# Performance work log

Measured on AMD Instinct MI355X. Metric: run time of the kernel, lower is better.

## Reference

```python
import jax, jax.numpy as jnp
import numpy as np

D_SPEC, D_PRE, D_CTX, D_H = 552, 256, 128, 1024


def _lstm_cell(x, h, c, Wih, Whh, bih, bhh):
    # PyTorch gate order: i, f, g, o
    g = x @ Wih.T + bih + h @ Whh.T + bhh
    i, f, gg, o = jnp.split(g, 4, axis=-1)
    c_new = jax.nn.sigmoid(f) * c + jax.nn.sigmoid(i) * jnp.tanh(gg)
    h_new = jax.nn.sigmoid(o) * jnp.tanh(c_new)
    return h_new, c_new


def _conv1d(x, w, b):
    # x: [B, C_in, L], w: [C_out, C_in, K], 'same' padding for K=5
    y = jax.lax.conv_general_dilated(x, w, window_strides=(1,), padding=[(2, 2)],
                                     dimension_numbers=('NCH', 'OIH', 'NCH'))
    return y + b[None, :, None]


def setup_inputs() -> dict:
    key = jax.random.key(0)
    ks = jax.random.split(key, 26)
    s = 0.05
    shapes = {
        'S_pad': (600, 64, D_SPEC),
        'pre_W1': (D_PRE, D_SPEC), 'pre_b1': (D_PRE,),
        'pre_W2': (D_PRE, D_PRE), 'pre_b2': (D_PRE,),
        'Wih0': (4 * D_H, D_PRE + D_CTX), 'Whh0': (4 * D_H, D_H),
        'bih0': (4 * D_H,), 'bhh0': (4 * D_H,),
        'Wih1': (4 * D_H, D_H), 'Whh1': (4 * D_H, D_H),
        'bih1': (4 * D_H,), 'bhh1': (4 * D_H,),
        'lin_W': (D_SPEC, D_H + D_CTX), 'lin_b': (D_SPEC,),
        'cw1': (512, D_SPEC, 5), 'cb1': (512,),
        'cw2': (512, 512, 5), 'cb2': (512,),
        'cw3': (512, 512, 5), 'cb3': (512,),
        'cw4': (512, 512, 5), 'cb4': (512,),
        'cw5': (D_SPEC, 512, 5), 'cb5': (D_SPEC,),
    }
    out = {}
    for i, (name, shp) in enumerate(shapes.items()):
        scale = 1.0 if name == 'S_pad' else s
        out[name] = scale * jax.random.normal(ks[i], shp, dtype=jnp.float32)
    return out


def reference(S_pad, pre_W1, pre_b1, pre_W2, pre_b2,
              Wih0, Whh0, bih0, bhh0, Wih1, Whh1, bih1, bhh1,
              lin_W, lin_b, cw1, cb1, cw2, cb2, cw3, cb3, cw4, cb4, cw5, cb5):
    L, B, _ = S_pad.shape
    # teacher forcing: input frame at t is S_pad[t-1] (zeros at t=0) -> precompute pre_net batched
    in_frames = jnp.concatenate([jnp.zeros((1, B, D_SPEC), S_pad.dtype), S_pad[:-1]], axis=0)
    pre = jax.nn.relu(in_frames @ pre_W1.T + pre_b1)
    pre = jax.nn.relu(pre @ pre_W2.T + pre_b2)  # dropout = identity (eval)
    ctx = jnp.zeros((L, B, D_CTX), S_pad.dtype)  # dummy_context
    lstm_in = jnp.concatenate([pre, ctx], axis=-1)  # [L, B, 384]

    h0 = jnp.zeros((B, D_H), S_pad.dtype)
    init = (h0, h0, h0, h0)  # (h0, c0, h1, c1)

    def step(carry, x):
        h0, c0, h1, c1 = carry
        h0, c0 = _lstm_cell(x, h0, c0, Wih0, Whh0, bih0, bhh0)
        h1, c1 = _lstm_cell(h0, h1, c1, Wih1, Whh1, bih1, bhh1)
        return (h0, c0, h1, c1), h1

    _, outs = jax.lax.scan(step, init, lstm_in)  # [L, B, 1024]
    S_pred = jnp.concatenate([outs, ctx], axis=-1) @ lin_W.T + lin_b  # [L, B, 552]

    x = jnp.transpose(S_pred, (1, 2, 0))  # [B, 552, L]
    x = jnp.tanh(_conv1d(x, cw1, cb1))
    x = jnp.tanh(_conv1d(x, cw2, cb2))
    x = jnp.tanh(_conv1d(x, cw3, cb3))
    x = jnp.tanh(_conv1d(x, cw4, cb4))
    x = _conv1d(x, cw5, cb5)
    S_residual = jnp.transpose(x, (2, 0, 1))  # [L, B, 552]
    return S_pred + S_residual
```

## Files before the change

kernel.cpp:

```cpp
#include <hip/hip_runtime.h>
#include <cstdint>
#include <cstddef>

typedef __bf16 bf16;
typedef __attribute__((ext_vector_type(8))) __bf16 bf16x8;
typedef __attribute__((ext_vector_type(4))) float f32x4;

#define DEV static __device__ __forceinline__

DEV float sigm_(float x) { return 1.f / (1.f + __expf(-x)); }
DEV float tanhf_(float x) {
  float e = __expf(-2.f * fabsf(x));
  float t = (1.f - e) / (1.f + e);
  return x < 0.f ? -t : t;
}

DEV void gload_lds16(const bf16* g, bf16* l) {
  __builtin_amdgcn_global_load_lds((const __attribute__((address_space(1))) void*)g,
                                   (__attribute__((address_space(3))) void*)l, 16, 0, 0);
}

__global__ void k_frames(const float* __restrict__ S, bf16* __restrict__ dst) {
  int idx = blockIdx.x * 256 + threadIdx.x;
  if (idx >= 38400 * 576) return;
  int r = idx / 576, c = idx - r * 576;
  int t = r >> 6, b = r & 63;
  float v = (t == 0 || c >= 552) ? 0.f : S[((size_t)(t - 1) * 64 + b) * 552 + c];
  dst[idx] = (bf16)v;
}

__global__ void k_pad2d(const float* __restrict__ src, bf16* __restrict__ dst,
                        int N, int Cdst, int Csrc, int Rsrc, int sstride) {
  int idx = blockIdx.x * 256 + threadIdx.x;
  if (idx >= N) return;
  int r = idx / Cdst, c = idx - r * Cdst;
  float v = (r < Rsrc && c < Csrc) ? src[(size_t)r * sstride + c] : 0.f;
  dst[idx] = (bf16)v;
}

__global__ void k_w0c(const float* __restrict__ Whh0, const float* __restrict__ Wih0,
                      bf16* __restrict__ dst) {
  int idx = blockIdx.x * 256 + threadIdx.x;
  if (idx >= 4096 * 1280) return;
  int r = idx / 1280, k = idx - r * 1280;
  float v = (k < 1024) ? Whh0[(size_t)r * 1024 + k] : Wih0[(size_t)r * 384 + (k - 1024)];
  dst[idx] = (bf16)v;
}

__global__ void k_w1c(const float* __restrict__ Wih1, const float* __restrict__ Whh1,
                      bf16* __restrict__ dst) {
  int idx = blockIdx.x * 256 + threadIdx.x;
  if (idx >= 4096 * 2048) return;
  int r = idx / 2048, k = idx - r * 2048;
  float v = (k < 1024) ? Wih1[(size_t)r * 1024 + k] : Whh1[(size_t)r * 1024 + (k - 1024)];
  dst[idx] = (bf16)v;
}

__global__ void k_convw(const float* __restrict__ src, bf16* __restrict__ dst,
                        int N, int Cpad, int Cisrc, int Cosrc) {
  int idx = blockIdx.x * 256 + threadIdx.x;
  if (idx >= N) return;
  int per = 5 * Cpad;
  int co = idx / per, rem = idx - co * per;
  int tap = rem / Cpad, ci = rem - tap * Cpad;
  float v = (co < Cosrc && ci < Cisrc) ? src[((size_t)co * Cisrc + ci) * 5 + tap] : 0.f;
  dst[idx] = (bf16)v;
}

__global__ void k_zpad(bf16* __restrict__ X0, bf16* __restrict__ X1, bf16* __restrict__ X2) {
  int idx = blockIdx.x * 256 + threadIdx.x;
  if (idx >= 64 * 4 * 1600) return;
  int per = 4 * 1600;
  int b = idx / per, rem = idx - b * per;
  int rr = rem / 1600, c = rem - rr * 1600;
  int row = (rr < 2) ? rr : 600 + rr;
  if (c < 576) X0[((size_t)b * 604 + row) * 576 + c] = (bf16)0.f;
  else if (c < 1088) X1[((size_t)b * 604 + row) * 512 + (c - 576)] = (bf16)0.f;
  else X2[((size_t)b * 604 + row) * 512 + (c - 1088)] = (bf16)0.f;
}

enum { M_RELU = 0, M_LINEAR = 1, M_CONVT = 2, M_CONVF = 3 };

template <int MODE>
__global__ __launch_bounds__(256) void gemm_k(
    const bf16* __restrict__ A, const bf16* __restrict__ B, int Ktot, int Kstride,
    int Brows, const float* __restrict__ bias,
    bf16* __restrict__ outB, int outStride, int colP, int colOff,
    float* __restrict__ outF, bf16* __restrict__ outX) {
  const int tid = threadIdx.x;
  const int lane = tid & 63, wv = tid >> 6;
  const int n0 = blockIdx.x * 128, m0 = blockIdx.y * 128;
  const int bz = blockIdx.z;
  __shared__ bf16 As[128 * 64];
  __shared__ bf16 Bs[128 * 64];
  f32x4 acc[4][4] = {};
  const int wr = wv >> 1, wc = wv & 1;
  int tap = 0, ci0 = 0;

  for (int kb = 0; kb < Ktot; kb += 64) {
#pragma unroll
    for (int j = 0; j < 4; ++j) {
      int rt = wv * 32 + j * 8 + (lane >> 3);
      const bf16* gp;
      if (MODE == M_CONVT || MODE == M_CONVF) {
        int l = m0 + rt;
        if (l > 599) l = 599;
        gp = A + ((size_t)(bz * 604 + l + tap)) * Kstride + ci0 + (lane & 7) * 8;
      } else {
        gp = A + (size_t)(m0 + rt) * Kstride + kb + (lane & 7) * 8;
      }
      gload_lds16(gp, &As[(wv * 32 + j * 8) * 64]);
    }
#pragma unroll
    for (int j = 0; j < 4; ++j) {
      int rn = n0 + wv * 32 + j * 8 + (lane >> 3);
      if (rn >= Brows) rn = Brows - 1;
      const bf16* gp = B + (size_t)rn * Ktot + kb + (lane & 7) * 8;
      gload_lds16(gp, &Bs[(wv * 32 + j * 8) * 64]);
    }
    __syncthreads();
#pragma unroll
    for (int ks = 0; ks < 2; ++ks) {
      const int ko = ks * 32 + (lane >> 4) * 8;
      bf16x8 af[4], bfr[4];
#pragma unroll
      for (int i = 0; i < 4; ++i) {
        af[i] = *(const bf16x8*)&As[(wr * 64 + i * 16 + (lane & 15)) * 64 + ko];
        bfr[i] = *(const bf16x8*)&Bs[(wc * 64 + i * 16 + (lane & 15)) * 64 + ko];
      }
#pragma unroll
      for (int mi = 0; mi < 4; ++mi)
#pragma unroll
        for (int ni = 0; ni < 4; ++ni)
          acc[mi][ni] = __builtin_amdgcn_mfma_f32_16x16x32_bf16(af[mi], bfr[ni], acc[mi][ni], 0, 0, 0);
    }
    __syncthreads();
    ci0 += 64;
    if (ci0 == Kstride) { ci0 = 0; ++tap; }
  }

  const int r0 = (lane >> 4) * 4, cc = lane & 15;
#pragma unroll
  for (int mi = 0; mi < 4; ++mi) {
#pragma unroll
    for (int ni = 0; ni < 4; ++ni) {
#pragma unroll
      for (int r = 0; r < 4; ++r) {
        float v = acc[mi][ni][r];
        int gr = m0 + wr * 64 + mi * 16 + r0 + r;
        int gc = n0 + wc * 64 + ni * 16 + cc;
        if (MODE == M_RELU) {
          v += bias[gc];
          v = fmaxf(v, 0.f);
          outB[(size_t)(gr >> 6) * outStride + (size_t)(gr & 63) * colP + colOff + gc] = (bf16)v;
        } else if (MODE == M_LINEAR) {
          if (gc < 552) {
            v += bias[gc];
            int t = gr >> 6, b = gr & 63;
            outF[(size_t)gr * 552 + gc] = v;
            outX[((size_t)b * 604 + t + 2) * 576 + gc] = (bf16)v;
          }
        } else if (MODE == M_CONVT) {
          if (gr < 600) {
            v = tanhf_(v + bias[gc]);
            outB[((size_t)bz * 604 + gr + 2) * 512 + gc] = (bf16)v;
          }
        } else {
          if (gr < 600 && gc < 552) {
            v += bias[gc];
            float* p = outF + ((size_t)gr * 64 + bz) * 552 + gc;
            *p += v;
          }
        }
      }
    }
  }
}

template <int LAYER>
DEV void scan_impl(bf16* __restrict__ C0, bf16* __restrict__ H1,
                   const bf16* __restrict__ W, const float* __restrict__ bi,
                   const float* __restrict__ bh, unsigned* __restrict__ flags,
                   float* gb, int u0, int b0, int mh, int ub) {
  constexpr int KT = LAYER ? 2048 : 1280;
  constexpr int NKS = LAYER ? 16 : 10;
  const int tid = threadIdx.x, lane = tid & 63, w = tid >> 6;
  const int kb = w * (KT / 4);

  bf16x8 wreg[4][NKS];
#pragma unroll
  for (int gi = 0; gi < 4; ++gi)
#pragma unroll
    for (int ks = 0; ks < NKS; ++ks)
      wreg[gi][ks] = *(const bf16x8*)(W + (size_t)(gi * 1024 + u0 + (lane & 15)) * KT +
                                      kb + ks * 32 + (lane >> 4) * 8);

  const int bl = tid >> 3, uu = (tid & 7) * 2;
  float bs[4][2];
#pragma unroll
  for (int g = 0; g < 4; ++g)
#pragma unroll
    for (int j = 0; j < 2; ++j) {
      int rw = g * 1024 + u0 + uu + j;
      bs[g][j] = bi[rw] + bh[rw];
    }
  float cst[2] = {0.f, 0.f};

  unsigned* flO = flags + (LAYER * 2 + mh) * 64 * 32;
  unsigned* flP = flags + mh * 64 * 32;

  const int r0 = lane & 15, q8 = (lane >> 4) * 8;

  for (int t = 0; t < 600; ++t) {
    if (w == 0 && (LAYER || t > 0)) {
      const unsigned tO = (unsigned)t, tP = (unsigned)(t + 1);
      for (;;) {
        bool bad = __hip_atomic_load(&flO[lane << 5], __ATOMIC_RELAXED, __HIP_MEMORY_SCOPE_AGENT) < tO;
        if (LAYER)
          bad |= __hip_atomic_load(&flP[lane << 5], __ATOMIC_RELAXED, __HIP_MEMORY_SCOPE_AGENT) < tP;
        if (!__ballot(bad)) break;
        __builtin_amdgcn_s_sleep(1);
      }
    }
    __syncthreads();

    const bf16* A0;
    int RS;
    if (!LAYER) {
      RS = 1280;
      A0 = C0 + (size_t)t * 81920 + (size_t)(b0 + r0) * 1280 + kb + q8;
    } else if (w < 2) {
      RS = 1280;
      A0 = C0 + (size_t)(t + 1) * 81920 + (size_t)(b0 + r0) * 1280 + w * 512 + q8;
    } else {
      RS = 1024;
      A0 = H1 + (size_t)(t + 1) * 65536 + (size_t)(b0 + r0) * 1024 + (w - 2) * 512 + q8;
    }
    const bf16* A1 = A0 + 16 * RS;

    f32x4 acc[4][2] = {};
#pragma unroll
    for (int ks = 0; ks < NKS; ++ks) {
      bf16x8 a0 = *(const bf16x8*)(A0 + ks * 32);
      bf16x8 a1 = *(const bf16x8*)(A1 + ks * 32);
#pragma unroll
      for (int gi = 0; gi < 4; ++gi) {
        acc[gi][0] = __builtin_amdgcn_mfma_f32_16x16x32_bf16(a0, wreg[gi][ks], acc[gi][0], 0, 0, 0);
        acc[gi][1] = __builtin_amdgcn_mfma_f32_16x16x32_bf16(a1, wreg[gi][ks], acc[gi][1], 0, 0, 0);
      }
    }

    const int un = lane & 15, qb = (lane >> 4) * 4;
#pragma unroll
    for (int gi = 0; gi < 4; ++gi)
#pragma unroll
      for (int b2 = 0; b2 < 2; ++b2)
        *(f32x4*)&gb[((w * 4 + gi) * 16 + un) * 36 + b2 * 16 + qb] = acc[gi][b2];
    __syncthreads();

    float hv[2];
#pragma unroll
    for (int j = 0; j < 2; ++j) {
      const int u = uu + j;
      float s[4];
#pragma unroll
      for (int g = 0; g < 4; ++g) {
        float acc_s = 0.f;
#pragma unroll
        for (int ww = 0; ww < 4; ++ww) acc_s += gb[((ww * 4 + g) * 16 + u) * 36 + bl];
        s[g] = acc_s + bs[g][j];
      }
      float c = sigm_(s[1]) * cst[j] + sigm_(s[0]) * tanhf_(s[2]);
      cst[j] = c;
      hv[j] = sigm_(s[3]) * tanhf_(c);
    }
    union { bf16 h2[2]; unsigned u32; } pk;
    pk.h2[0] = (bf16)hv[0];
    pk.h2[1] = (bf16)hv[1];
    unsigned* dst =
        LAYER ? (unsigned*)(H1 + (size_t)(t + 2) * 65536 + (size_t)(b0 + bl) * 1024 + u0 + uu)
              : (unsigned*)(C0 + (size_t)(t + 1) * 81920 + (size_t)(b0 + bl) * 1280 + u0 + uu);
    __hip_atomic_store(dst, pk.u32, __ATOMIC_RELAXED, __HIP_MEMORY_SCOPE_AGENT);
    asm volatile("s_waitcnt vmcnt(0)" ::: "memory");
    __syncthreads();
    if (tid == 0)
      __hip_atomic_store(&flO[ub << 5], (unsigned)(t + 1), __ATOMIC_RELAXED, __HIP_MEMORY_SCOPE_AGENT);
  }
}

__global__ __launch_bounds__(256, 1) void lstm_k(
    bf16* __restrict__ C0, bf16* __restrict__ H1,
    const bf16* __restrict__ W0, const bf16* __restrict__ W1,
    const float* __restrict__ bi0, const float* __restrict__ bh0,
    const float* __restrict__ bi1, const float* __restrict__ bh1,
    unsigned* __restrict__ flags) {
  __shared__ float gb[256 * 36];
  const int bid = blockIdx.x;
  const int layer = bid >> 7, sub = bid & 127;
  const int mh = sub >> 6, ub = sub & 63;
  const int u0 = ub * 16, b0 = mh * 32;
  if (layer == 0)
    scan_impl<0>(C0, H1, W0, bi0, bh0, flags, gb, u0, b0, mh, ub);
  else
    scan_impl<1>(C0, H1, W1, bi1, bh1, flags, gb, u0, b0, mh, ub);
}

static inline unsigned gdiv(size_t n) { return (unsigned)((n + 255) / 256); }

extern "C" void kernel_launch(void* const* d_in, const int* in_sizes, int n_in,
                              void* d_out, int out_size, void* d_ws, size_t ws_size,
                              hipStream_t stream) {
  const float* S = (const float*)d_in[0];
  const float* preW1 = (const float*)d_in[1];
  const float* preb1 = (const float*)d_in[2];
  const float* preW2 = (const float*)d_in[3];
  const float* preb2 = (const float*)d_in[4];
  const float* Wih0 = (const float*)d_in[5];
  const float* Whh0 = (const float*)d_in[6];
  const float* bih0 = (const float*)d_in[7];
  const float* bhh0 = (const float*)d_in[8];
  const float* Wih1 = (const float*)d_in[9];
  const float* Whh1 = (const float*)d_in[10];
  const float* bih1 = (const float*)d_in[11];
  const float* bhh1 = (const float*)d_in[12];
  const float* linW = (const float*)d_in[13];
  const float* linb = (const float*)d_in[14];
  const float* cw1 = (const float*)d_in[15];
  const float* cb1 = (const float*)d_in[16];
  const float* cw2 = (const float*)d_in[17];
  const float* cb2 = (const float*)d_in[18];
  const float* cw3 = (const float*)d_in[19];
  const float* cb3 = (const float*)d_in[20];
  const float* cw4 = (const float*)d_in[21];
  const float* cb4 = (const float*)d_in[22];
  const float* cw5 = (const float*)d_in[23];
  const float* cb5 = (const float*)d_in[24];
  float* out = (float*)d_out;

  char* ws = (char*)d_ws;
  size_t off = 0;
  auto alloc = [&](size_t bytes) -> char* {
    char* p = ws + off;
    off += (bytes + 255) & ~(size_t)255;
    return p;
  };
  unsigned* flags = (unsigned*)alloc(32768);
  bf16* H1 = (bf16*)alloc(602ull * 64 * 1024 * 2);
  bf16* frames = (bf16*)alloc(38400ull * 576 * 2);
  bf16* pre1 = (bf16*)alloc(38400ull * 256 * 2);
  bf16* W0c = (bf16*)alloc(4096ull * 1280 * 2);
  bf16* W1c = (bf16*)alloc(4096ull * 2048 * 2);
  bf16* pW1b = (bf16*)alloc(256ull * 576 * 2);
  bf16* pW2b = (bf16*)alloc(256ull * 256 * 2);
  bf16* linWb = (bf16*)alloc(576ull * 1024 * 2);
  bf16* c1r = (bf16*)alloc(512ull * 5 * 576 * 2);
  bf16* c2r = (bf16*)alloc(512ull * 5 * 512 * 2);
  bf16* c3r = (bf16*)alloc(512ull * 5 * 512 * 2);
  bf16* c4r = (bf16*)alloc(512ull * 5 * 512 * 2);
  bf16* c5r = (bf16*)alloc(576ull * 5 * 512 * 2);
  bf16* X0 = (bf16*)alloc(64ull * 604 * 576 * 2);
  bf16* X1 = (bf16*)alloc(64ull * 604 * 512 * 2);
  bf16* X2 = (bf16*)alloc(64ull * 604 * 512 * 2);
  bf16* C0 = X0;

  hipMemsetAsync(ws, 0, 32768 + 2ull * 64 * 1024 * 2, stream);
  hipMemsetAsync(C0, 0, 64ull * 1280 * 2, stream);

  k_frames<<<gdiv(38400ull * 576), 256, 0, stream>>>(S, frames);
  k_pad2d<<<gdiv(256 * 576), 256, 0, stream>>>(preW1, pW1b, 256 * 576, 576, 552, 256, 552);
  k_pad2d<<<gdiv(256 * 256), 256, 0, stream>>>(preW2, pW2b, 256 * 256, 256, 256, 256, 256);
  k_pad2d<<<gdiv(576 * 1024), 256, 0, stream>>>(linW, linWb, 576 * 1024, 1024, 1024, 552, 1152);
  k_w0c<<<gdiv(4096ull * 1280), 256, 0, stream>>>(Whh0, Wih0, W0c);
  k_w1c<<<gdiv(4096ull * 2048), 256, 0, stream>>>(Wih1, Whh1, W1c);
  k_convw<<<gdiv(512ull * 5 * 576), 256, 0, stream>>>(cw1, c1r, 512 * 5 * 576, 576, 552, 512);
  k_convw<<<gdiv(512ull * 5 * 512), 256, 0, stream>>>(cw2, c2r, 512 * 5 * 512, 512, 512, 512);
  k_convw<<<gdiv(512ull * 5 * 512), 256, 0, stream>>>(cw3, c3r, 512 * 5 * 512, 512, 512, 512);
  k_convw<<<gdiv(512ull * 5 * 512), 256, 0, stream>>>(cw4, c4r, 512 * 5 * 512, 512, 512, 512);
  k_convw<<<gdiv(576ull * 5 * 512), 256, 0, stream>>>(cw5, c5r, 576 * 5 * 512, 512, 512, 552);

  gemm_k<M_RELU><<<dim3(2, 300, 1), 256, 0, stream>>>(frames, pW1b, 576, 576, 256, preb1,
                                                      pre1, 16384, 256, 0, nullptr, nullptr);
  gemm_k<M_RELU><<<dim3(2, 300, 1), 256, 0, stream>>>(pre1, pW2b, 256, 256, 256, preb2,
                                                      C0, 81920, 1280, 1024, nullptr, nullptr);
  lstm_k<<<dim3(256), 256, 0, stream>>>(C0, H1, W0c, W1c, bih0, bhh0, bih1, bhh1, flags);
  k_zpad<<<gdiv(64 * 4 * 1600), 256, 0, stream>>>(X0, X1, X2);
  gemm_k<M_LINEAR><<<dim3(5, 300, 1), 256, 0, stream>>>(H1 + 131072, linWb, 1024, 1024, 576, linb,
                                                        nullptr, 0, 0, 0, out, X0);
  gemm_k<M_CONVT><<<dim3(4, 5, 64), 256, 0, stream>>>(X0, c1r, 2880, 576, 512, cb1,
                                                      X1, 0, 0, 0, nullptr, nullptr);
  gemm_k<M_CONVT><<<dim3(4, 5, 64), 256, 0, stream>>>(X1, c2r, 2560, 512, 512, cb2,
                                                      X2, 0, 0, 0, nullptr, nullptr);
  gemm_k<M_CONVT><<<dim3(4, 5, 64), 256, 0, stream>>>(X2, c3r, 2560, 512, 512, cb3,
                                                      X1, 0, 0, 0, nullptr, nullptr);
  gemm_k<M_CONVT><<<dim3(4, 5, 64), 256, 0, stream>>>(X1, c4r, 2560, 512, 512, cb4,
                                                      X2, 0, 0, 0, nullptr, nullptr);
  gemm_k<M_CONVF><<<dim3(5, 5, 64), 256, 0, stream>>>(X2, c5r, 2560, 512, 576, cb5,
                                                      nullptr, 0, 0, 0, out, nullptr);
  (void)in_sizes; (void)n_in; (void)out_size; (void)ws_size;
}
```

Measured before the change: 6.056 ms.

## Replace LSTM flag handshake with sentinel-polling on data and double wave count

The persistent LSTM kernel no longer uses per-block progress flags. Each hidden-state buffer is pre-filled with 0xFFFF sentinels, and consumers spin on cache-bypassing loads of the activations until no sentinel remains. The loaded values then feed the MFMAs directly. The block also grows from 4 to 8 waves, halving each wave's K slice and weight registers, and h values are packed four per 64-bit store. The intent is to cut the flag write/poll round-trip and the extra barriers per timestep. The risk is that 0xFFFFFFFF could in principle be a real bf16 pair (a NaN pattern), and polling full data vectors adds memory traffic.

Result: faster. 5.133 ms (-15.2%).

```diff
diff --git a/kernel.cpp b/kernel.cpp
--- a/kernel.cpp
+++ b/kernel.cpp
@@ -5,6 +5,7 @@
 typedef __bf16 bf16;
 typedef __attribute__((ext_vector_type(8))) __bf16 bf16x8;
 typedef __attribute__((ext_vector_type(4))) float f32x4;
+typedef __attribute__((ext_vector_type(4))) unsigned u32x4;
 
 #define DEV static __device__ __forceinline__
 
@@ -77,6 +78,15 @@
   if (c < 576) X0[((size_t)b * 604 + row) * 576 + c] = (bf16)0.f;
   else if (c < 1088) X1[((size_t)b * 604 + row) * 512 + (c - 576)] = (bf16)0.f;
   else X2[((size_t)b * 604 + row) * 512 + (c - 1088)] = (bf16)0.f;
+}
+
+__global__ void k_sent(unsigned* __restrict__ C0u) {
+  int idx = blockIdx.x * 256 + threadIdx.x;
+  if (idx >= 600 * 64 * 512) return;
+  int d = idx & 511;
+  int rb = idx >> 9;
+  int b = rb & 63, t1 = (rb >> 6) + 1;
+  C0u[(size_t)t1 * 40960 + (size_t)b * 640 + d] = 0xFFFFFFFFu;
 }
 
 enum { M_RELU = 0, M_LINEAR = 1, M_CONVT = 2, M_CONVF = 3 };
@@ -180,12 +190,11 @@
 template <int LAYER>
 DEV void scan_impl(bf16* __restrict__ C0, bf16* __restrict__ H1,
                    const bf16* __restrict__ W, const float* __restrict__ bi,
-                   const float* __restrict__ bh, unsigned* __restrict__ flags,
-                   float* gb, int u0, int b0, int mh, int ub) {
+                   const float* __restrict__ bh, float* gb, int u0, int b0) {
   constexpr int KT = LAYER ? 2048 : 1280;
-  constexpr int NKS = LAYER ? 16 : 10;
+  constexpr int NKS = KT / 256;
   const int tid = threadIdx.x, lane = tid & 63, w = tid >> 6;
-  const int kb = w * (KT / 4);
+  const int kb = w * (KT / 8);
 
   bf16x8 wreg[4][NKS];
 #pragma unroll
@@ -195,54 +204,71 @@
       wreg[gi][ks] = *(const bf16x8*)(W + (size_t)(gi * 1024 + u0 + (lane & 15)) * KT +
                                       kb + ks * 32 + (lane >> 4) * 8);
 
-  const int bl = tid >> 3, uu = (tid & 7) * 2;
-  float bs[4][2];
-#pragma unroll
-  for (int g = 0; g < 4; ++g)
-#pragma unroll
-    for (int j = 0; j < 2; ++j) {
-      int rw = g * 1024 + u0 + uu + j;
-      bs[g][j] = bi[rw] + bh[rw];
-    }
-  float cst[2] = {0.f, 0.f};
-
-  unsigned* flO = flags + (LAYER * 2 + mh) * 64 * 32;
-  unsigned* flP = flags + mh * 64 * 32;
+  const int uc = tid & 15, bl = tid >> 4;
+  float bs[4];
+#pragma unroll
+  for (int g = 0; g < 4; ++g) bs[g] = bi[g * 1024 + u0 + uc] + bh[g * 1024 + u0 + uc];
+  float cst = 0.f;
+  const int rotc = (bl + 4 * uc) & 31;
 
   const int r0 = lane & 15, q8 = (lane >> 4) * 8;
+  const int un = lane & 15, qb = (lane >> 4) * 4;
 
   for (int t = 0; t < 600; ++t) {
-    if (w == 0 && (LAYER || t > 0)) {
-      const unsigned tO = (unsigned)t, tP = (unsigned)(t + 1);
-      for (;;) {
-        bool bad = __hip_atomic_load(&flO[lane << 5], __ATOMIC_RELAXED, __HIP_MEMORY_SCOPE_AGENT) < tO;
-        if (LAYER)
-          bad |= __hip_atomic_load(&flP[lane << 5], __ATOMIC_RELAXED, __HIP_MEMORY_SCOPE_AGENT) < tP;
-        if (!__ballot(bad)) break;
-        __builtin_amdgcn_s_sleep(1);
-      }
-    }
-    __syncthreads();
-
     const bf16* A0;
     int RS;
     if (!LAYER) {
       RS = 1280;
       A0 = C0 + (size_t)t * 81920 + (size_t)(b0 + r0) * 1280 + kb + q8;
-    } else if (w < 2) {
+    } else if (w < 4) {
       RS = 1280;
-      A0 = C0 + (size_t)(t + 1) * 81920 + (size_t)(b0 + r0) * 1280 + w * 512 + q8;
+      A0 = C0 + (size_t)(t + 1) * 81920 + (size_t)(b0 + r0) * 1280 + kb + q8;
     } else {
       RS = 1024;
-      A0 = H1 + (size_t)(t + 1) * 65536 + (size_t)(b0 + r0) * 1024 + (w - 2) * 512 + q8;
+      A0 = H1 + (size_t)(t + 1) * 65536 + (size_t)(b0 + r0) * 1024 + (kb - 1024) + q8;
     }
     const bf16* A1 = A0 + 16 * RS;
 
+    u32x4 va[NKS], vb[NKS];
+    if (!LAYER) {
+#pragma unroll
+      for (int ks = 0; ks < NKS; ++ks)
+        if (kb + ks * 32 >= 1024) {
+          va[ks] = *(const u32x4*)(A0 + ks * 32);
+          vb[ks] = *(const u32x4*)(A1 + ks * 32);
+        }
+    }
+    for (;;) {
+#pragma unroll
+      for (int ks = 0; ks < NKS; ++ks) {
+        if (LAYER || kb + ks * 32 < 1024) {
+          asm volatile("global_load_dwordx4 %0, %1, off sc0 sc1"
+                       : "=v"(va[ks]) : "v"(A0 + ks * 32) : "memory");
+          asm volatile("global_load_dwordx4 %0, %1, off sc0 sc1"
+                       : "=v"(vb[ks]) : "v"(A1 + ks * 32) : "memory");
+        }
+      }
+      asm volatile("s_waitcnt vmcnt(0)" ::: "memory");
+      __builtin_amdgcn_sched_barrier(0);
+      unsigned bad = 0;
+#pragma unroll
+      for (int ks = 0; ks < NKS; ++ks) {
+        if (LAYER || kb + ks * 32 < 1024) {
+          bad |= (va[ks].x == 0xFFFFFFFFu) | (va[ks].y == 0xFFFFFFFFu) |
+                 (va[ks].z == 0xFFFFFFFFu) | (va[ks].w == 0xFFFFFFFFu) |
+                 (vb[ks].x == 0xFFFFFFFFu) | (vb[ks].y == 0xFFFFFFFFu) |
+                 (vb[ks].z == 0xFFFFFFFFu) | (vb[ks].w == 0xFFFFFFFFu);
+        }
+      }
+      if (!__ballot(bad)) break;
+      __builtin_amdgcn_s_sleep(2);
+    }
+
     f32x4 acc[4][2] = {};
 #pragma unroll
     for (int ks = 0; ks < NKS; ++ks) {
-      bf16x8 a0 = *(const bf16x8*)(A0 + ks * 32);
-      bf16x8 a1 = *(const bf16x8*)(A1 + ks * 32);
+      bf16x8 a0 = *(const bf16x8*)&va[ks];
+      bf16x8 a1 = *(const bf16x8*)&vb[ks];
 #pragma unroll
       for (int gi = 0; gi < 4; ++gi) {
         acc[gi][0] = __builtin_amdgcn_mfma_f32_16x16x32_bf16(a0, wreg[gi][ks], acc[gi][0], 0, 0, 0);
@@ -250,59 +276,58 @@
       }
     }
 
-    const int un = lane & 15, qb = (lane >> 4) * 4;
 #pragma unroll
     for (int gi = 0; gi < 4; ++gi)
 #pragma unroll
       for (int b2 = 0; b2 < 2; ++b2)
-        *(f32x4*)&gb[((w * 4 + gi) * 16 + un) * 36 + b2 * 16 + qb] = acc[gi][b2];
-    __syncthreads();
-
-    float hv[2];
-#pragma unroll
-    for (int j = 0; j < 2; ++j) {
-      const int u = uu + j;
-      float s[4];
-#pragma unroll
-      for (int g = 0; g < 4; ++g) {
-        float acc_s = 0.f;
-#pragma unroll
-        for (int ww = 0; ww < 4; ++ww) acc_s += gb[((ww * 4 + g) * 16 + u) * 36 + bl];
-        s[g] = acc_s + bs[g][j];
-      }
-      float c = sigm_(s[1]) * cst[j] + sigm_(s[0]) * tanhf_(s[2]);
-      cst[j] = c;
-      hv[j] = sigm_(s[3]) * tanhf_(c);
-    }
-    union { bf16 h2[2]; unsigned u32; } pk;
-    pk.h2[0] = (bf16)hv[0];
-    pk.h2[1] = (bf16)hv[1];
-    unsigned* dst =
-        LAYER ? (unsigned*)(H1 + (size_t)(t + 2) * 65536 + (size_t)(b0 + bl) * 1024 + u0 + uu)
-              : (unsigned*)(C0 + (size_t)(t + 1) * 81920 + (size_t)(b0 + bl) * 1280 + u0 + uu);
-    __hip_atomic_store(dst, pk.u32, __ATOMIC_RELAXED, __HIP_MEMORY_SCOPE_AGENT);
-    asm volatile("s_waitcnt vmcnt(0)" ::: "memory");
-    __syncthreads();
-    if (tid == 0)
-      __hip_atomic_store(&flO[ub << 5], (unsigned)(t + 1), __ATOMIC_RELAXED, __HIP_MEMORY_SCOPE_AGENT);
+        *(f32x4*)&gb[((w * 4 + gi) * 16 + un) * 32 + ((b2 * 16 + qb + 4 * un) & 31)] = acc[gi][b2];
+
+    asm volatile("s_waitcnt lgkmcnt(0)" ::: "memory");
+    __builtin_amdgcn_s_barrier();
+    __builtin_amdgcn_sched_barrier(0);
+
+    float s4[4];
+#pragma unroll
+    for (int g = 0; g < 4; ++g) {
+      float a = 0.f;
+#pragma unroll
+      for (int ww = 0; ww < 8; ++ww) a += gb[((ww * 4 + g) * 16 + uc) * 32 + rotc];
+      s4[g] = a + bs[g];
+    }
+    float c = sigm_(s4[1]) * cst + sigm_(s4[0]) * tanhf_(s4[2]);
+    cst = c;
+    float h = sigm_(s4[3]) * tanhf_(c);
+
+    float h1 = __shfl_down(h, 1), h2 = __shfl_down(h, 2), h3 = __shfl_down(h, 3);
+    if ((uc & 3) == 0) {
+      union { bf16 q[4]; unsigned long long u; } pk;
+      pk.q[0] = (bf16)h; pk.q[1] = (bf16)h1; pk.q[2] = (bf16)h2; pk.q[3] = (bf16)h3;
+      unsigned long long* dst = LAYER
+          ? (unsigned long long*)(H1 + (size_t)(t + 2) * 65536 + (size_t)(b0 + bl) * 1024 + u0 + uc)
+          : (unsigned long long*)(C0 + (size_t)(t + 1) * 81920 + (size_t)(b0 + bl) * 1280 + u0 + uc);
+      __hip_atomic_store(dst, pk.u, __ATOMIC_RELAXED, __HIP_MEMORY_SCOPE_AGENT);
+    }
+
+    asm volatile("s_waitcnt lgkmcnt(0)" ::: "memory");
+    __builtin_amdgcn_s_barrier();
+    __builtin_amdgcn_sched_barrier(0);
   }
 }
 
-__global__ __launch_bounds__(256, 1) void lstm_k(
+__global__ __launch_bounds__(512, 1) void lstm_k(
     bf16* __restrict__ C0, bf16* __restrict__ H1,
     const bf16* __restrict__ W0, const bf16* __restrict__ W1,
     const float* __restrict__ bi0, const float* __restrict__ bh0,
-    const float* __restrict__ bi1, const float* __restrict__ bh1,
-    unsigned* __restrict__ flags) {
-  __shared__ float gb[256 * 36];
+    const float* __restrict__ bi1, const float* __restrict__ bh1) {
+  __shared__ float gb[512 * 32];
   const int bid = blockIdx.x;
   const int layer = bid >> 7, sub = bid & 127;
   const int mh = sub >> 6, ub = sub & 63;
   const int u0 = ub * 16, b0 = mh * 32;
   if (layer == 0)
-    scan_impl<0>(C0, H1, W0, bi0, bh0, flags, gb, u0, b0, mh, ub);
+    scan_impl<0>(C0, H1, W0, bi0, bh0, gb, u0, b0);
   else
-    scan_impl<1>(C0, H1, W1, bi1, bh1, flags, gb, u0, b0, mh, ub);
+    scan_impl<1>(C0, H1, W1, bi1, bh1, gb, u0, b0);
 }
 
 static inline unsigned gdiv(size_t n) { return (unsigned)((n + 255) / 256); }
@@ -344,7 +369,6 @@
     off += (bytes + 255) & ~(size_t)255;
     return p;
   };
-  unsigned* flags = (unsigned*)alloc(32768);
   bf16* H1 = (bf16*)alloc(602ull * 64 * 1024 * 2);
   bf16* frames = (bf16*)alloc(38400ull * 576 * 2);
   bf16* pre1 = (bf16*)alloc(38400ull * 256 * 2);
@@ -363,8 +387,10 @@
   bf16* X2 = (bf16*)alloc(64ull * 604 * 512 * 2);
   bf16* C0 = X0;
 
-  hipMemsetAsync(ws, 0, 32768 + 2ull * 64 * 1024 * 2, stream);
+  hipMemsetAsync(H1, 0, 2ull * 64 * 1024 * 2, stream);
+  hipMemsetAsync((char*)H1 + 2ull * 64 * 1024 * 2, 0xFF, 600ull * 64 * 1024 * 2, stream);
   hipMemsetAsync(C0, 0, 64ull * 1280 * 2, stream);
+  k_sent<<<gdiv(600ull * 64 * 512), 256, 0, stream>>>((unsigned*)C0);
 
   k_frames<<<gdiv(38400ull * 576), 256, 0, stream>>>(S, frames);
   k_pad2d<<<gdiv(256 * 576), 256, 0, stream>>>(preW1, pW1b, 256 * 576, 576, 552, 256, 552);
@@ -382,7 +408,7 @@
                                                       pre1, 16384, 256, 0, nullptr, nullptr);
   gemm_k<M_RELU><<<dim3(2, 300, 1), 256, 0, stream>>>(pre1, pW2b, 256, 256, 256, preb2,
                                                       C0, 81920, 1280, 1024, nullptr, nullptr);
-  lstm_k<<<dim3(256), 256, 0, stream>>>(C0, H1, W0c, W1c, bih0, bhh0, bih1, bhh1, flags);
+  lstm_k<<<dim3(256), 512, 0, stream>>>(C0, H1, W0c, W1c, bih0, bhh0, bih1, bhh1);
   k_zpad<<<gdiv(64 * 4 * 1600), 256, 0, stream>>>(X0, X1, X2);
   gemm_k<M_LINEAR><<<dim3(5, 300, 1), 256, 0, stream>>>(H1 + 131072, linWb, 1024, 1024, 576, linb,
                                                         nullptr, 0, 0, 0, out, X0);
```
